# Kernel tuning notes

Hardware: AMD Instinct MI355X
Metric: run time of the kernel (lower is better)

Reference implementation:

```python
import jax, jax.numpy as jnp
import numpy as np
import math

H = 16
D_MODEL = 1024
D_K = D_MODEL // H  # 64
B = 4
S = 2048
D_V = 64


def setup_inputs() -> dict:
    key0 = jax.random.key(0)
    ks = jax.random.split(key0, 7)
    scale = 1.0 / math.sqrt(D_MODEL)
    return {
        "query": jax.random.normal(ks[0], (B, S, D_MODEL), jnp.float32),
        "key": jax.random.normal(ks[1], (B, S, D_MODEL), jnp.float32),
        "value": jax.random.normal(ks[2], (B, D_V, S), jnp.float32),
        "Wq": jax.random.normal(ks[3], (D_MODEL, D_MODEL), jnp.float32) * scale,
        "bq": jax.random.normal(ks[4], (D_MODEL,), jnp.float32) * scale,
        "Wk": jax.random.normal(ks[5], (D_MODEL, D_MODEL), jnp.float32) * scale,
        "bk": jax.random.normal(ks[6], (D_MODEL,), jnp.float32) * scale,
    }


def reference(query, key, value, Wq, bq, Wk, bk):
    nb = query.shape[0]
    # Linear projections then split heads: [B,S,d_model] -> [B,h,S,d_k]
    q = (query @ Wq.T + bq).reshape(nb, -1, H, D_K).transpose(0, 2, 1, 3)
    k = (key @ Wk.T + bk).reshape(nb, -1, H, D_K).transpose(0, 2, 1, 3)
    # value.repeat(h,1,1,1).permute(1,0,3,2): [B,dv,Sk] -> broadcast over heads
    # with last two axes swapped -> effectively v[b,s,d] = value[b,d,s]
    v = jnp.swapaxes(value, 1, 2)  # [B, Sk, dv]
    # Scaled dot-product attention (mask branch is a no-op: m == zeros)
    scores = jnp.einsum("bhqd,bhkd->bhqk", q, k) / math.sqrt(D_K)
    p_attn = jax.nn.softmax(scores, axis=-1)
    # value identical across heads, contract directly with base v
    x = jnp.einsum("bhqk,bkd->bhqd", p_attn, v)  # [B,h,Sq,dv]
    return (jnp.mean(x, axis=1), q)
```

## Files before the change

kernel.cpp:

```cpp
#include <hip/hip_runtime.h>


typedef unsigned short u16;
typedef __attribute__((ext_vector_type(8))) u16 u16x8;
typedef __attribute__((ext_vector_type(8))) __bf16 bf16x8;
typedef __attribute__((ext_vector_type(4))) float f32x4;
typedef __attribute__((ext_vector_type(16))) float f32x16;
typedef __attribute__((ext_vector_type(2))) unsigned u32x2;
typedef __attribute__((ext_vector_type(4))) unsigned u32x4;

typedef const __attribute__((address_space(1))) void gvoid;
typedef __attribute__((address_space(3))) void lvoid;

__device__ __forceinline__ void gload16(const void* g, void* l) {
  __builtin_amdgcn_global_load_lds((gvoid*)g, (lvoid*)l, 16, 0, 0);
}

__device__ __forceinline__ u16 f2bf(float f) {
  unsigned u = __builtin_bit_cast(unsigned, f);
  u += 0x7fffu + ((u >> 16) & 1u);
  return (u16)(u >> 16);
}

__device__ __forceinline__ unsigned cvtpk(float lo, float hi) {
  unsigned r;
  asm("v_cvt_pk_bf16_f32 %0, %1, %2" : "=v"(r) : "v"(lo), "v"(hi));
  return r;
}

__device__ __forceinline__ float exp2a(float x) {
  float r;
  asm("v_exp_f32 %0, %1" : "=v"(r) : "v"(x));
  return r;
}

__device__ __forceinline__ f32x16 zero16() {
  f32x16 z;
#pragma unroll
  for (int i = 0; i < 16; ++i) z[i] = 0.f;
  return z;
}

#define MFMA_PV(D, A, B) \
  asm("s_nop 1\n\tv_mfma_f32_32x32x16_bf16 %0, %1, %2, %0" : "+v"(D) : "v"(A), "v"(B))
#define MFMA_DRAIN_V(X) asm("s_nop 7\n\ts_nop 7\n\ts_nop 4" : "+v"(X))

#define SOFTMAX_CVT(P, PF0, PF1, LACC)                                               \
  {                                                                                  \
    _Pragma("unroll")                                                                \
    for (int r = 0; r < 16; ++r) P[r] = exp2a(P[r]);                                 \
    LACC += (((P[0]+P[1])+(P[2]+P[3])) + ((P[4]+P[5])+(P[6]+P[7])))                  \
          + (((P[8]+P[9])+(P[10]+P[11])) + ((P[12]+P[13])+(P[14]+P[15])));           \
    u32x2 sA0 = __builtin_amdgcn_permlane32_swap(cvtpk(P[0],P[1]),   cvtpk(P[4],P[5]),   false,false); \
    u32x2 sB0 = __builtin_amdgcn_permlane32_swap(cvtpk(P[2],P[3]),   cvtpk(P[6],P[7]),   false,false); \
    u32x2 sA1 = __builtin_amdgcn_permlane32_swap(cvtpk(P[8],P[9]),   cvtpk(P[12],P[13]), false,false); \
    u32x2 sB1 = __builtin_amdgcn_permlane32_swap(cvtpk(P[10],P[11]), cvtpk(P[14],P[15]), false,false); \
    u32x4 w0_{sA0[0], sB0[0], sA0[1], sB0[1]};                                       \
    u32x4 w1_{sA1[0], sB1[0], sA1[1], sB1[1]};                                       \
    PF0 = __builtin_bit_cast(bf16x8, w0_);                                           \
    PF1 = __builtin_bit_cast(bf16x8, w1_);                                           \
  }

#define ST_BLOCK(ST)                                                                 \
  {                                                                                  \
    f32x16 p = zero16();                                                             \
    __builtin_amdgcn_s_setprio(1);                                                   \
    _Pragma("unroll")                                                                \
    for (int c = 0; c < 4; ++c) {                                                    \
      int ka = bo + ((((ST * 32 + l31) * 128) + c * 32 + hi * 16) ^ xm);             \
      bf16x8 kf = __builtin_bit_cast(bf16x8, *reinterpret_cast<const u16x8*>(KtB + ka)); \
      MFMA_PV(p, kf, aq[c]);                                                         \
    }                                                                                \
    __builtin_amdgcn_s_setprio(0);                                                   \
    MFMA_DRAIN_V(p);            \
    bf16x8 pf0, pf1;                                                                 \
    SOFTMAX_CVT(p, pf0, pf1, lA);                                                    \
    _Pragma("unroll")                                                                \
    for (int kc = 0; kc < 2; ++kc) {                                                 \
      int cb = ST * 64 + kc * 32 + hi * 16;                                          \
      bf16x8 vA = __builtin_bit_cast(bf16x8,                                         \
          *reinterpret_cast<const u16x8*>(VtB + bo + ((l31 * 128 + cb) ^ xm)));      \
      bf16x8 vB = __builtin_bit_cast(bf16x8,                                         \
          *reinterpret_cast<const u16x8*>(VtB + bo + (((32 + l31) * 128 + cb) ^ xm))); \
      bf16x8 pf = kc ? pf1 : pf0;                                                    \
      __builtin_amdgcn_s_setprio(1);                                                 \
      oA = __builtin_amdgcn_mfma_f32_32x32x16_bf16(vA, pf, oA, 0, 0, 0);             \
      oB = __builtin_amdgcn_mfma_f32_32x32x16_bf16(vB, pf, oB, 0, 0, 0);             \
      __builtin_amdgcn_s_setprio(0);                                                 \
    }                                                                                \
  }

__global__ __launch_bounds__(256, 4) void attn_kernel(
    const float* __restrict__ qf, const u16* __restrict__ k_ws,
    const u16* __restrict__ valb, u16* __restrict__ x_ws)
{
  const int wgid = (blockIdx.x & 7) * 128 + (blockIdx.x >> 3);
  const int qblk = wgid & 15;
  const int h = (wgid >> 4) & 15;
  const int b = wgid >> 8;
  const int bh = b * 16 + h;

  const int tid = threadIdx.x, lane = tid & 63, w = tid >> 6;
  const int l31 = lane & 31, hi = lane >> 5;
  const int xm = (lane & 7) << 4;

  __shared__ u16 Kt[2][4096];
  __shared__ u16 Vt[2][4096];
  char* KtB = (char*)&Kt[0][0];
  char* VtB = (char*)&Vt[0][0];

  bf16x8 aq[4];
  {
    const float qs = 0.125f * 1.4426950408889634f;
    const size_t qb0 = ((size_t)bh * 2048 + qblk * 128 + w * 32 + l31) * 64;
#pragma unroll
    for (int c = 0; c < 4; ++c) {
      const float* src = &qf[qb0 + c * 16 + hi * 8];
      float4 v0 = *reinterpret_cast<const float4*>(src);
      float4 v1 = *reinterpret_cast<const float4*>(src + 4);
      u16x8 t;
      t[0] = f2bf(v0.x * qs); t[1] = f2bf(v0.y * qs);
      t[2] = f2bf(v0.z * qs); t[3] = f2bf(v0.w * qs);
      t[4] = f2bf(v1.x * qs); t[5] = f2bf(v1.y * qs);
      t[6] = f2bf(v1.z * qs); t[7] = f2bf(v1.w * qs);
      aq[c] = __builtin_bit_cast(bf16x8, t);
    }
  }

  const u16* kg = k_ws + (size_t)bh * 131072;
  const u16* vg = valb + (size_t)b * 131072;
  const u16* ks0 = kg + (tid >> 3) * 64 + ((tid ^ (tid >> 3)) & 7) * 8;
  const u16* vs0 = vg + (tid >> 3) * 2048 + ((tid ^ (tid >> 3)) & 7) * 8;
  char* kd0 = (char*)Kt + w * 1024;
  char* vd0 = (char*)Vt + w * 1024;

  gload16(ks0, kd0);           gload16(ks0 + 2048, kd0 + 4096);
  gload16(vs0, vd0);           gload16(vs0 + 65536, vd0 + 4096);

  float lA = 0.0f;
  f32x16 oA = zero16(), oB = zero16();
  int cur = 0;
  __syncthreads();

  for (int t = 0; t < 32; ++t) {
    if (t < 31) {
      int nb = (cur ^ 1) * 8192;
      size_t ko = (size_t)(t + 1) * 4096;
      int vo = (t + 1) * 64;
      gload16(ks0 + ko, kd0 + nb);           gload16(ks0 + ko + 2048, kd0 + nb + 4096);
      gload16(vs0 + vo, vd0 + nb);           gload16(vs0 + vo + 65536, vd0 + nb + 4096);
    }
    const int bo = cur * 8192;

    ST_BLOCK(0)
    ST_BLOCK(1)

    __syncthreads();
    cur ^= 1;
  }

  float lr = lA + __shfl_xor(lA, 32);
  float inv = 1.0f / lr;
  size_t ob0 = ((size_t)bh * 2048 + qblk * 128 + w * 32 + l31) * 64;
#pragma unroll
  for (int g = 0; g < 4; ++g) {
    u32x2 aa{cvtpk(oA[g*4+0]*inv, oA[g*4+1]*inv), cvtpk(oA[g*4+2]*inv, oA[g*4+3]*inv)};
    u32x2 bb{cvtpk(oB[g*4+0]*inv, oB[g*4+1]*inv), cvtpk(oB[g*4+2]*inv, oB[g*4+3]*inv)};
    *reinterpret_cast<u32x2*>(&x_ws[ob0 + g * 8 + hi * 4]) = aa;
    *reinterpret_cast<u32x2*>(&x_ws[ob0 + 32 + g * 8 + hi * 4]) = bb;
  }
}

__global__ void cvt_small(const float* __restrict__ wq, const float* __restrict__ wk,
                          const float* __restrict__ v,
                          u16* __restrict__ wqb, u16* __restrict__ wkb, u16* __restrict__ vb) {
  int i = blockIdx.x * 256 + threadIdx.x;
  const float* s;
  u16* d;
  int off;
  if (i < 262144)      { s = wq; d = wqb; off = i; }
  else if (i < 524288) { s = wk; d = wkb; off = i - 262144; }
  else if (i < 655360) { s = v;  d = vb;  off = i - 524288; }
  else return;
  float4 x = reinterpret_cast<const float4*>(s)[off];
  ushort4 o;
  o.x = f2bf(x.x); o.y = f2bf(x.y); o.z = f2bf(x.z); o.w = f2bf(x.w);
  reinterpret_cast<ushort4*>(d)[off] = o;
}

__global__ __launch_bounds__(256) void proj_gemm(
    const float* __restrict__ qf, const float* __restrict__ kf,
    const u16* __restrict__ Wqb, const u16* __restrict__ Wkb,
    const float* __restrict__ bq, const float* __restrict__ bk,
    float* __restrict__ out1, u16* __restrict__ k_ws)
{
  const int z = blockIdx.z;
  const float* __restrict__ A = z ? kf : qf;
  const u16* __restrict__ W = z ? Wkb : Wqb;
  const float* __restrict__ bias = z ? bk : bq;

  __shared__ u16 As[2][128 * 64];
  __shared__ u16 Bs[2][128 * 64];

  const int tid = threadIdx.x;
  const int lane = tid & 63;
  const int w = tid >> 6;
  const int ln = lane & 15;
  const int lh = lane >> 4;
  const int wm = w >> 1, wn = w & 1;
  const int n0 = blockIdx.x * 128;
  const int j0 = blockIdx.y * 128;

  f32x4 acc[4][4];
#pragma unroll
  for (int mt = 0; mt < 4; ++mt)
#pragma unroll
    for (int nt = 0; nt < 4; ++nt)
      acc[mt][nt] = f32x4{0.f, 0.f, 0.f, 0.f};

  const int r_ = tid >> 3, c8_ = tid & 7;
  const int swz = c8_ ^ (r_ & 7);
  const int rxm = (ln & 7) << 3;

#pragma unroll
  for (int it = 0; it < 4; ++it)
    gload16(&W[(size_t)(j0 + it * 32 + r_) * 1024 + swz * 8], &Bs[0][(it * 256 + w * 64) * 8]);
#pragma unroll
  for (int j = 0; j < 4; ++j) {
    int u = tid + j * 256;
    int r = u >> 3;
    int sl = (u & 7) ^ (r & 7);
    const float* s = &A[(size_t)(n0 + r) * 1024 + (u & 7) * 8];
    float4 x0 = *reinterpret_cast<const float4*>(s);
    float4 x1 = *reinterpret_cast<const float4*>(s + 4);
    u32x4 wv{cvtpk(x0.x, x0.y), cvtpk(x0.z, x0.w), cvtpk(x1.x, x1.y), cvtpk(x1.z, x1.w)};
    *reinterpret_cast<u32x4*>(&As[0][r * 64 + sl * 8]) = wv;
  }
  __syncthreads();

  for (int kt = 0; kt < 16; ++kt) {
    const int cur = kt & 1, nb = cur ^ 1;
    float4 ax0[4], ax1[4];
    if (kt < 15) {
#pragma unroll
      for (int it = 0; it < 4; ++it)
        gload16(&W[(size_t)(j0 + it * 32 + r_) * 1024 + (kt + 1) * 64 + swz * 8],
                &Bs[nb][(it * 256 + w * 64) * 8]);
#pragma unroll
      for (int j = 0; j < 4; ++j) {
        int u = tid + j * 256;
        const float* s = &A[(size_t)(n0 + (u >> 3)) * 1024 + (kt + 1) * 64 + (u & 7) * 8];
        ax0[j] = *reinterpret_cast<const float4*>(s);
        ax1[j] = *reinterpret_cast<const float4*>(s + 4);
      }
    }
#pragma unroll
    for (int ks = 0; ks < 2; ++ks) {
      bf16x8 a[4], bfr[4];
#pragma unroll
      for (int mt = 0; mt < 4; ++mt) {
        int row = wm * 64 + mt * 16 + ln;
        a[mt] = __builtin_bit_cast(bf16x8,
            *reinterpret_cast<const u16x8*>(&As[cur][row * 64 + (((lh + ks * 4) * 8) ^ rxm)]));
      }
#pragma unroll
      for (int nt = 0; nt < 4; ++nt) {
        int row = wn * 64 + nt * 16 + ln;
        bfr[nt] = __builtin_bit_cast(bf16x8,
            *reinterpret_cast<const u16x8*>(&Bs[cur][row * 64 + (((lh + ks * 4) * 8) ^ rxm)]));
      }
      __builtin_amdgcn_s_setprio(1);
#pragma unroll
      for (int mt = 0; mt < 4; ++mt)
#pragma unroll
        for (int nt = 0; nt < 4; ++nt)
          acc[mt][nt] = __builtin_amdgcn_mfma_f32_16x16x32_bf16(a[mt], bfr[nt], acc[mt][nt], 0, 0, 0);
      __builtin_amdgcn_s_setprio(0);
    }
    if (kt < 15) {
#pragma unroll
      for (int j = 0; j < 4; ++j) {
        int u = tid + j * 256;
        int r = u >> 3;
        int sl = (u & 7) ^ (r & 7);
        u32x4 wv{cvtpk(ax0[j].x, ax0[j].y), cvtpk(ax0[j].z, ax0[j].w),
                 cvtpk(ax1[j].x, ax1[j].y), cvtpk(ax1[j].z, ax1[j].w)};
        *reinterpret_cast<u32x4*>(&As[nb][r * 64 + sl * 8]) = wv;
      }
      __syncthreads();
    }
  }

#pragma unroll
  for (int nt = 0; nt < 4; ++nt) {
    int j = j0 + wn * 64 + nt * 16 + ln;
    float bv = bias[j];
    int h = j >> 6, d = j & 63;
#pragma unroll
    for (int mt = 0; mt < 4; ++mt) {
#pragma unroll
      for (int r = 0; r < 4; ++r) {
        int n = n0 + wm * 64 + mt * 16 + lh * 4 + r;
        int bidx = n >> 11, s = n & 2047;
        size_t off = ((size_t)(bidx * 16 + h) * 2048 + s) * 64 + d;
        float val = acc[mt][nt][r] + bv;
        if (z == 0) out1[off] = val;
        else        k_ws[off] = f2bf(val);
      }
    }
  }
}

__global__ void mean_heads(const u16* __restrict__ x_ws, float* __restrict__ out0) {
  int i = blockIdx.x * 256 + threadIdx.x;
  int d0 = (i & 7) * 8;
  int s = (i >> 3) & 2047;
  int b = i >> 14;
  float acc[8];
#pragma unroll
  for (int j = 0; j < 8; ++j) acc[j] = 0.f;
#pragma unroll
  for (int h = 0; h < 16; ++h) {
    u16x8 v = *reinterpret_cast<const u16x8*>(
        &x_ws[(((size_t)(b * 16 + h) * 2048 + s) << 6) + d0]);
#pragma unroll
    for (int j = 0; j < 8; ++j)
      acc[j] += __builtin_bit_cast(float, (unsigned)v[j] << 16);
  }
  float4 o0{acc[0] * 0.0625f, acc[1] * 0.0625f, acc[2] * 0.0625f, acc[3] * 0.0625f};
  float4 o1{acc[4] * 0.0625f, acc[5] * 0.0625f, acc[6] * 0.0625f, acc[7] * 0.0625f};
  size_t ob = ((size_t)(b * 2048 + s) << 6) + d0;
  *reinterpret_cast<float4*>(&out0[ob]) = o0;
  *reinterpret_cast<float4*>(&out0[ob + 4]) = o1;
}

extern "C" void kernel_launch(void* const* d_in, const int* in_sizes, int n_in,
                              void* d_out, int out_size, void* d_ws, size_t ws_size,
                              hipStream_t stream) {
  (void)in_sizes; (void)n_in; (void)out_size; (void)ws_size;
  const float* query = (const float*)d_in[0];
  const float* key   = (const float*)d_in[1];
  const float* value = (const float*)d_in[2];
  const float* Wq    = (const float*)d_in[3];
  const float* bq    = (const float*)d_in[4];
  const float* Wk    = (const float*)d_in[5];
  const float* bk    = (const float*)d_in[6];

  float* out0 = (float*)d_out;
  float* out1 = out0 + 524288;

  char* ws = (char*)d_ws;
  const size_t MB = 1u << 20;
  u16* x_ws = (u16*)(ws + 0);
  u16* Wqb  = (u16*)(ws + 32 * MB);
  u16* Wkb  = (u16*)(ws + 34 * MB);
  u16* valb = (u16*)(ws + 36 * MB);
  u16* k_ws = (u16*)(ws + 37 * MB);

  cvt_small<<<2560, 256, 0, stream>>>(Wq, Wk, value, Wqb, Wkb, valb);
  proj_gemm<<<dim3(64, 8, 2), 256, 0, stream>>>(query, key, Wqb, Wkb, bq, bk, out1, k_ws);
  attn_kernel<<<1024, 256, 0, stream>>>(out1, k_ws, valb, x_ws);
  mean_heads<<<256, 256, 0, stream>>>(x_ws, out0);
}
```

Before: 153.2 us.

## Split attention output dims across two wave groups with 512-thread blocks

Doubles the block to 512 threads. Each pair of waves shares a 32-query slice, and each wave of the pair computes half of the 64 output value dimensions, so it holds one accumulator instead of two. Tile loads are spread over more threads, one load per thread per buffer. QK^T and the softmax are now computed twice, once per wave of each pair, in exchange for more waves in flight and fewer accumulator registers per wave.

```diff
diff --git a/kernel.cpp b/kernel.cpp
--- a/kernel.cpp
+++ b/kernel.cpp
@@ -78,19 +78,16 @@
     _Pragma("unroll")                                                                \
     for (int kc = 0; kc < 2; ++kc) {                                                 \
       int cb = ST * 64 + kc * 32 + hi * 16;                                          \
-      bf16x8 vA = __builtin_bit_cast(bf16x8,                                         \
-          *reinterpret_cast<const u16x8*>(VtB + bo + ((l31 * 128 + cb) ^ xm)));      \
-      bf16x8 vB = __builtin_bit_cast(bf16x8,                                         \
-          *reinterpret_cast<const u16x8*>(VtB + bo + (((32 + l31) * 128 + cb) ^ xm))); \
+      bf16x8 vD = __builtin_bit_cast(bf16x8,                                         \
+          *reinterpret_cast<const u16x8*>(VtB + bo + (((wd * 32 + l31) * 128 + cb) ^ xm))); \
       bf16x8 pf = kc ? pf1 : pf0;                                                    \
       __builtin_amdgcn_s_setprio(1);                                                 \
-      oA = __builtin_amdgcn_mfma_f32_32x32x16_bf16(vA, pf, oA, 0, 0, 0);             \
-      oB = __builtin_amdgcn_mfma_f32_32x32x16_bf16(vB, pf, oB, 0, 0, 0);             \
+      o16 = __builtin_amdgcn_mfma_f32_32x32x16_bf16(vD, pf, o16, 0, 0, 0);           \
       __builtin_amdgcn_s_setprio(0);                                                 \
     }                                                                                \
   }
 
-__global__ __launch_bounds__(256, 4) void attn_kernel(
+__global__ __launch_bounds__(512, 4) void attn_kernel(
     const float* __restrict__ qf, const u16* __restrict__ k_ws,
     const u16* __restrict__ valb, u16* __restrict__ x_ws)
 {
@@ -101,6 +98,7 @@
   const int bh = b * 16 + h;
 
   const int tid = threadIdx.x, lane = tid & 63, w = tid >> 6;
+  const int wq = w & 3, wd = w >> 2;
   const int l31 = lane & 31, hi = lane >> 5;
   const int xm = (lane & 7) << 4;
 
@@ -112,7 +110,7 @@
   bf16x8 aq[4];
   {
     const float qs = 0.125f * 1.4426950408889634f;
-    const size_t qb0 = ((size_t)bh * 2048 + qblk * 128 + w * 32 + l31) * 64;
+    const size_t qb0 = ((size_t)bh * 2048 + qblk * 128 + wq * 32 + l31) * 64;
 #pragma unroll
     for (int c = 0; c < 4; ++c) {
       const float* src = &qf[qb0 + c * 16 + hi * 8];
@@ -134,21 +132,19 @@
   char* kd0 = (char*)Kt + w * 1024;
   char* vd0 = (char*)Vt + w * 1024;
 
-  gload16(ks0, kd0);           gload16(ks0 + 2048, kd0 + 4096);
-  gload16(vs0, vd0);           gload16(vs0 + 65536, vd0 + 4096);
+  gload16(ks0, kd0);
+  gload16(vs0, vd0);
 
   float lA = 0.0f;
-  f32x16 oA = zero16(), oB = zero16();
+  f32x16 o16 = zero16();
   int cur = 0;
   __syncthreads();
 
   for (int t = 0; t < 32; ++t) {
     if (t < 31) {
       int nb = (cur ^ 1) * 8192;
-      size_t ko = (size_t)(t + 1) * 4096;
-      int vo = (t + 1) * 64;
-      gload16(ks0 + ko, kd0 + nb);           gload16(ks0 + ko + 2048, kd0 + nb + 4096);
-      gload16(vs0 + vo, vd0 + nb);           gload16(vs0 + vo + 65536, vd0 + nb + 4096);
+      gload16(ks0 + (size_t)(t + 1) * 4096, kd0 + nb);
+      gload16(vs0 + (t + 1) * 64, vd0 + nb);
     }
     const int bo = cur * 8192;
 
@@ -161,13 +157,11 @@
 
   float lr = lA + __shfl_xor(lA, 32);
   float inv = 1.0f / lr;
-  size_t ob0 = ((size_t)bh * 2048 + qblk * 128 + w * 32 + l31) * 64;
+  size_t ob0 = ((size_t)bh * 2048 + qblk * 128 + wq * 32 + l31) * 64 + wd * 32;
 #pragma unroll
   for (int g = 0; g < 4; ++g) {
-    u32x2 aa{cvtpk(oA[g*4+0]*inv, oA[g*4+1]*inv), cvtpk(oA[g*4+2]*inv, oA[g*4+3]*inv)};
-    u32x2 bb{cvtpk(oB[g*4+0]*inv, oB[g*4+1]*inv), cvtpk(oB[g*4+2]*inv, oB[g*4+3]*inv)};
+    u32x2 aa{cvtpk(o16[g*4+0]*inv, o16[g*4+1]*inv), cvtpk(o16[g*4+2]*inv, o16[g*4+3]*inv)};
     *reinterpret_cast<u32x2*>(&x_ws[ob0 + g * 8 + hi * 4]) = aa;
-    *reinterpret_cast<u32x2*>(&x_ws[ob0 + 32 + g * 8 + hi * 4]) = bb;
   }
 }
 
@@ -359,6 +353,6 @@
 
   cvt_small<<<2560, 256, 0, stream>>>(Wq, Wk, value, Wqb, Wkb, valb);
   proj_gemm<<<dim3(64, 8, 2), 256, 0, stream>>>(query, key, Wqb, Wkb, bq, bk, out1, k_ws);
-  attn_kernel<<<1024, 256, 0, stream>>>(out1, k_ws, valb, x_ws);
+  attn_kernel<<<1024, 512, 0, stream>>>(out1, k_ws, valb, x_ws);
   mean_heads<<<256, 256, 0, stream>>>(x_ws, out0);
 }
```

Result: slower. 199.1 us (+29.9%).
